# Performance work log

Hardware: AMD Instinct MI355X
Metric: run time of the kernel (lower is better)

The kernel has to match this reference:

```python
import jax, jax.numpy as jnp
import numpy as np

H = 128      # hidden_sizes
E = 128      # embedding_size
V = 100000   # n_words
C = 10       # n_classes
B, S, L = 32, 32, 64
PAD = 0


def _gru_dir(x, w_ih, w_hh, b_ih, b_hh, reverse):
    # x: [N, T, D]; torch GRU cell convention (r, z, n gate order)
    xp = jnp.einsum('ntd,gd->ntg', x, w_ih) + b_ih  # [N, T, 3H]
    if reverse:
        xp = xp[:, ::-1]
    h0 = jnp.zeros((x.shape[0], w_hh.shape[1]), x.dtype)

    def step(h, xt):
        gh = h @ w_hh.T + b_hh
        xr, xz, xn = jnp.split(xt, 3, axis=-1)
        hr, hz, hn = jnp.split(gh, 3, axis=-1)
        r = jax.nn.sigmoid(xr + hr)
        z = jax.nn.sigmoid(xz + hz)
        n = jnp.tanh(xn + r * hn)
        h2 = (1.0 - z) * n + z * h
        return h2, h2

    _, hs = jax.lax.scan(step, h0, jnp.swapaxes(xp, 0, 1))
    hs = jnp.swapaxes(hs, 0, 1)  # [N, T, H]
    if reverse:
        hs = hs[:, ::-1]
    return hs


def _bi_gru(x, pf, pb):
    return jnp.concatenate([_gru_dir(x, *pf, False), _gru_dir(x, *pb, True)], axis=-1)


def _attn_pool(h, W, b, ctx):
    # h: [N, T, 2H] -> pooled [N, 2H]
    u = jnp.tanh(jnp.einsum('ntd,ed->nte', h, W) + b)
    a = jax.nn.softmax(u @ ctx, axis=1)          # [N, T]
    return jnp.einsum('ntd,nt->nd', h, a)


def setup_inputs() -> dict:
    key = jax.random.key(0)
    ks = jax.random.split(key, 24)
    sc = 0.05
    d = {}
    d['X'] = jax.random.randint(ks[0], (B, S, L), 0, V, dtype=jnp.int32)
    d['emb'] = jax.random.normal(ks[1], (V, E), jnp.float32) * sc
    # word-level bi-GRU (input E)
    d['w_ih_f'] = jax.random.normal(ks[2], (3 * H, E), jnp.float32) * sc
    d['w_hh_f'] = jax.random.normal(ks[3], (3 * H, H), jnp.float32) * sc
    d['b_ih_f'] = jnp.zeros((3 * H,), jnp.float32)
    d['b_hh_f'] = jnp.zeros((3 * H,), jnp.float32)
    d['w_ih_b'] = jax.random.normal(ks[4], (3 * H, E), jnp.float32) * sc
    d['w_hh_b'] = jax.random.normal(ks[5], (3 * H, H), jnp.float32) * sc
    d['b_ih_b'] = jnp.zeros((3 * H,), jnp.float32)
    d['b_hh_b'] = jnp.zeros((3 * H,), jnp.float32)
    d['Ww'] = jax.random.normal(ks[6], (2 * H, 2 * H), jnp.float32) * sc
    d['bw'] = jnp.zeros((2 * H,), jnp.float32)
    d['ctx_w'] = jax.random.normal(ks[7], (2 * H,), jnp.float32) * sc
    # sentence-level bi-GRU (input 2H)
    d['s_ih_f'] = jax.random.normal(ks[8], (3 * H, 2 * H), jnp.float32) * sc
    d['s_hh_f'] = jax.random.normal(ks[9], (3 * H, H), jnp.float32) * sc
    d['sb_ih_f'] = jnp.zeros((3 * H,), jnp.float32)
    d['sb_hh_f'] = jnp.zeros((3 * H,), jnp.float32)
    d['s_ih_b'] = jax.random.normal(ks[10], (3 * H, 2 * H), jnp.float32) * sc
    d['s_hh_b'] = jax.random.normal(ks[11], (3 * H, H), jnp.float32) * sc
    d['sb_ih_b'] = jnp.zeros((3 * H,), jnp.float32)
    d['sb_hh_b'] = jnp.zeros((3 * H,), jnp.float32)
    d['Ws'] = jax.random.normal(ks[12], (2 * H, 2 * H), jnp.float32) * sc
    d['bs'] = jnp.zeros((2 * H,), jnp.float32)
    d['ctx_s'] = jax.random.normal(ks[13], (2 * H,), jnp.float32) * sc
    d['Wc'] = jax.random.normal(ks[14], (C, 2 * H), jnp.float32) * sc
    d['bc'] = jnp.zeros((C,), jnp.float32)
    return d


def reference(X, emb, w_ih_f, w_hh_f, b_ih_f, b_hh_f, w_ih_b, w_hh_b, b_ih_b, b_hh_b,
              Ww, bw, ctx_w, s_ih_f, s_hh_f, sb_ih_f, sb_hh_f, s_ih_b, s_hh_b,
              sb_ih_b, sb_hh_b, Ws, bs, ctx_s, Wc, bc):
    emb = emb.at[PAD].set(0.0)               # padding_idx semantics
    words = emb[X.reshape(B * S, L)]          # [B*S, L, E]
    h_w = _bi_gru(words, (w_ih_f, w_hh_f, b_ih_f, b_hh_f),
                  (w_ih_b, w_hh_b, b_ih_b, b_hh_b))  # [B*S, L, 2H]
    sents = _attn_pool(h_w, Ww, bw, ctx_w).reshape(B, S, 2 * H)
    h_s = _bi_gru(sents, (s_ih_f, s_hh_f, sb_ih_f, sb_hh_f),
                  (s_ih_b, s_hh_b, sb_ih_b, sb_hh_b))  # [B, S, 2H]
    doc = _attn_pool(h_s, Ws, bs, ctx_s)      # [B, 2H]
    return doc @ Wc.T + bc                    # [B, C]
```

## Files before the change

### kernel.cpp

```cpp
#include <hip/hip_runtime.h>
#include <hip/hip_bf16.h>
#include <math.h>

#define Bd 32
#define Sd 32
#define Ld 64
#define Ed 128
#define Hd 128
#define MW 65536
#define MS 1024

#define OFF_WIHT_S   0
#define OFF_WFW_W    196608
#define OFF_WFW_S    262144
#define OFF_W6       327680
#define OFF_BIH_W    622592
#define OFF_BIH_S    623360
#define OFF_BHH_W    624128
#define OFF_BHH_S    624896
#define OFF_WFX      625664
#define OFF_HW       723968
#define OFF_SENTS    17763328
#define OFF_XP_S     18025472
#define OFF_HS       18811904
#define OFF_DOC      19078144
#define OFF_WFHH     19086336
#define WS_FLOATS    19184640

typedef __attribute__((ext_vector_type(8))) short sh8;
typedef __attribute__((ext_vector_type(4))) float f32x4;
typedef unsigned short u16;
typedef unsigned int u32;

#define GLD  388
#define XPLD 385
#define HPLD 520

__device__ __forceinline__ void barrier_lds_only() {
    asm volatile("s_waitcnt lgkmcnt(0)\n\ts_barrier" ::: "memory");
}

__device__ __forceinline__ float sigmoidf_(float x) {
    return __fdividef(1.0f, 1.0f + __expf(-x));
}
__device__ __forceinline__ float tanhf_(float x) {
    float t = __expf(-2.0f * fabsf(x));
    float r = __fdividef(1.0f - t, 1.0f + t);
    return copysignf(r, x);
}
__device__ __forceinline__ u16 bf16_hi(float f) {
    u32 x = __float_as_uint(f);
    return (u16)((x + 0x7fffu + ((x >> 16) & 1u)) >> 16);
}
__device__ __forceinline__ float bf16_f(u16 u) { return __uint_as_float(((u32)u) << 16); }
__device__ __forceinline__ void bf16_split(float f, u16& hi, u16& lo) {
    hi = bf16_hi(f);
    lo = bf16_hi(f - bf16_f(hi));
}

__global__ void prep(const float* __restrict__ s_ih_f, const float* __restrict__ s_ih_b,
                     const float* __restrict__ w_ih_f, const float* __restrict__ w_ih_b,
                     const float* __restrict__ w_hh_f, const float* __restrict__ w_hh_b,
                     const float* __restrict__ s_hh_f, const float* __restrict__ s_hh_b,
                     const float* __restrict__ b_ih_f, const float* __restrict__ b_ih_b,
                     const float* __restrict__ sb_ih_f, const float* __restrict__ sb_ih_b,
                     const float* __restrict__ b_hh_f, const float* __restrict__ b_hh_b,
                     const float* __restrict__ sb_hh_f, const float* __restrict__ sb_hh_b,
                     float* __restrict__ ws)
{
    int i = blockIdx.x * 256 + threadIdx.x;
    if (i < 196608) {
        int k = i / 768, g = i % 768;
        ws[OFF_WIHT_S + i] = (g < 384) ? s_ih_f[g*256 + k] : s_ih_b[(g-384)*256 + k];
        return;
    }
    i -= 196608;
    if (i < 131072) return;
    i -= 131072;
    if (i < 294912) {
        int set = i / 49152, rem = i % 49152;
        int k4 = rem / 1536, r2 = rem % 1536, g = r2 >> 2, sub = r2 & 3;
        const float* w = (set==0) ? w_ih_f : (set==1) ? w_ih_b : (set==2) ? w_hh_f
                       : (set==3) ? w_hh_b : (set==4) ? s_hh_f : s_hh_b;
        ws[OFF_W6 + i] = w[g*128 + k4*4 + sub];
        return;
    }
    i -= 294912;
    if (i < 768) { ws[OFF_BIH_W + i] = (i<384) ? b_ih_f[i] : b_ih_b[i-384]; return; }
    i -= 768;
    if (i < 768) { ws[OFF_BIH_S + i] = (i<384) ? sb_ih_f[i] : sb_ih_b[i-384]; return; }
    i -= 768;
    if (i < 768) { ws[OFF_BHH_W + i] = (i<384) ? b_hh_f[i] : b_hh_b[i-384]; return; }
    i -= 768;
    if (i < 768) { ws[OFF_BHH_S + i] = (i<384) ? sb_hh_f[i] : sb_hh_b[i-384]; return; }
}

__global__ void prep2(const float* __restrict__ w_hh_f, const float* __restrict__ w_hh_b,
                      u16* __restrict__ WFo)
{
    int i = blockIdx.x * 256 + threadIdx.x;
    int within = i % 49152;
    int combo  = i / 49152;
    int half = combo & 1, dir = combo >> 1;
    int nt  = within / 2048;
    int r2  = within % 2048;
    int q   = r2 >> 9;
    int r3  = r2 & 511;
    int l   = r3 >> 3, e = r3 & 7;
    int n = nt*16 + (l & 15);
    int k = q*32 + ((l >> 4) << 3) + e;
    const float* src = dir ? w_hh_b : w_hh_f;
    float v = src[n*128 + k];
    u16 hi = bf16_hi(v);
    WFo[i] = half ? bf16_hi(v - bf16_f(hi)) : hi;
}

__global__ void prep3(const float* __restrict__ Ww, const float* __restrict__ Ws,
                      const float* __restrict__ w_ih_f, const float* __restrict__ w_ih_b,
                      u16* __restrict__ WFW_W, u16* __restrict__ WFW_S,
                      u16* __restrict__ WFX)
{
    int i = blockIdx.x * 256 + threadIdx.x;
    if (i < 262144) {
        int which = i / 131072;
        int w = i % 131072;
        int half = w / 65536;
        int r = w % 65536;
        int nt = r / 4096;
        int r2 = r % 4096;
        int q = r2 / 512;
        int l = (r2 % 512) >> 3, e = r2 & 7;
        int n = nt*16 + (l & 15);
        int k = q*32 + ((l >> 4) << 3) + e;
        const float* src = which ? Ws : Ww;
        float v = src[n*256 + k];
        u16 hi = bf16_hi(v);
        u16 o = half ? bf16_hi(v - bf16_f(hi)) : hi;
        (which ? WFW_S : WFW_W)[w] = o;
        return;
    }
    i -= 262144;
    if (i < 196608) {
        int w = i % 98304;
        int dir = i / 98304;
        int half = w / 49152;
        int r = w % 49152;
        int nt = r / 2048;
        int r2 = r % 2048;
        int q = r2 / 512;
        int l = (r2 % 512) >> 3, e = r2 & 7;
        int n = nt*16 + (l & 15);
        int k = q*32 + ((l >> 4) << 3) + e;
        const float* src = dir ? w_ih_b : w_ih_f;
        float v = src[n*128 + k];
        u16 hi = bf16_hi(v);
        WFX[i] = half ? bf16_hi(v - bf16_f(hi)) : hi;
        return;
    }
}

__global__ __launch_bounds__(768)
void gru_word_full(const int* __restrict__ X, const float* __restrict__ emb,
                   const u16* __restrict__ WFX, const u16* __restrict__ WFHH,
                   const float* __restrict__ b_ih_f, const float* __restrict__ b_ih_b,
                   const float* __restrict__ b_hh_f, const float* __restrict__ b_hh_b,
                   u16* __restrict__ houtp)
{
    const int bx = blockIdx.x;
    const int dir = bx >> 7;
    const int blk = bx & 127;
    const int seq0 = blk * 8;
    const int tid = threadIdx.x;
    const int lane = tid & 63;
    const int wid = tid >> 6;

    __shared__ float xp_lds[64 * XPLD];
    __shared__ f32x4 uni4[2048];
    __shared__ u16 h_pk[4 * HPLD];
    __shared__ int ids_s[8][64];
    float* G = (float*)uni4;
    u16* a_pk = (u16*)uni4;

    const int j = tid & 127;
    const int sg = tid >> 7;
    const bool gthread = tid < 512;
    const float* bih = dir ? b_ih_b : b_ih_f;
    const float* bhh = dir ? b_hh_b : b_hh_f;
    float bhr = 0.f, bhz = 0.f, bhn = 0.f;
    if (gthread) { bhr = bhh[j]; bhz = bhh[128 + j]; bhn = bhh[256 + j]; }

    const u16* WXbase = WFX + (long)dir * 98304;
    const u16* WHbase = WFHH + (long)dir * 98304;
    const int nt0 = wid*2, nt1 = wid*2 + 1;
    const int c0 = nt0*16 + (lane & 15);
    const int c1 = nt1*16 + (lane & 15);
    const int qj = j >> 5, subkj = (j >> 3) & 3, ej = j & 7;

    for (int i = tid; i < 512; i += 768)
        ids_s[i >> 6][i & 63] = X[(long)(seq0 + (i >> 6))*64 + (i & 63)];
    for (int i = tid; i < 4*HPLD; i += 768) h_pk[i] = 0;
    __syncthreads();

    float hprev0 = 0.f, hprev1 = 0.f;
    for (int c = 0; c < 8; ++c) {
        asm volatile("" ::: "memory");
        sh8 xh0[4], xl0[4], xh1[4], xl1[4];
#pragma unroll
        for (int q = 0; q < 4; ++q) {
            xh0[q] = *(const sh8*)(WXbase + (nt0*4 + q)*512 + lane*8);
            xl0[q] = *(const sh8*)(WXbase + 49152 + (nt0*4 + q)*512 + lane*8);
            xh1[q] = *(const sh8*)(WXbase + (nt1*4 + q)*512 + lane*8);
            xl1[q] = *(const sh8*)(WXbase + 49152 + (nt1*4 + q)*512 + lane*8);
        }
        const float bv0 = bih[c0], bv1 = bih[c1];
        for (int idx = tid; idx < 2048; idx += 768) {
            int cc2 = idx & 1, rm = (idx >> 1) & 7, subk = (idx >> 4) & 3;
            int q = (idx >> 6) & 3, mfs = idx >> 8;
            int ts = c*8 + rm;
            int t = dir ? 63 - ts : ts;
            int kk = q*32 + subk*8 + cc2*4;
            int id = ids_s[mfs][t];
            float4 v = make_float4(0.f, 0.f, 0.f, 0.f);
            if (id != 0) v = *(const float4*)&emb[(long)id*128 + kk];
            u16 h0,l0,h1,l1,h2,l2,h3,l3;
            bf16_split(v.x,h0,l0); bf16_split(v.y,h1,l1);
            bf16_split(v.z,h2,l2); bf16_split(v.w,h3,l3);
            int lh = subk*16 + rm;
            int base = (mfs*4 + q)*512 + lh*8 + cc2*4;
            uint2 whi = make_uint2((u32)h0 | ((u32)h1 << 16), (u32)h2 | ((u32)h3 << 16));
            uint2 wlo = make_uint2((u32)l0 | ((u32)l1 << 16), (u32)l2 | ((u32)l3 << 16));
            *(uint2*)&a_pk[base]      = whi;
            *(uint2*)&a_pk[base + 64] = wlo;
        }
        barrier_lds_only();
#pragma unroll
        for (int mf = 0; mf < 8; ++mf) {
            f32x4 A0 = (f32x4){0.f,0.f,0.f,0.f};
            f32x4 A1 = (f32x4){0.f,0.f,0.f,0.f};
#pragma unroll
            for (int q = 0; q < 4; ++q) {
                sh8 a = *(const sh8*)&a_pk[(mf*4 + q)*512 + lane*8];
                A0 = __builtin_amdgcn_mfma_f32_16x16x32_bf16(a, xh0[q], A0, 0,0,0);
                A0 = __builtin_amdgcn_mfma_f32_16x16x32_bf16(a, xl0[q], A0, 0,0,0);
                A1 = __builtin_amdgcn_mfma_f32_16x16x32_bf16(a, xh1[q], A1, 0,0,0);
                A1 = __builtin_amdgcn_mfma_f32_16x16x32_bf16(a, xl1[q], A1, 0,0,0);
            }
            float g0[4], g1[4];
#pragma unroll
            for (int r = 0; r < 4; ++r) {
                g0[r] = A0[r] + __shfl_xor(A0[r], 32);
                g1[r] = A1[r] + __shfl_xor(A1[r], 32);
            }
            if ((lane >= 32) == (mf & 1)) {
                int row = mf*8 + ((lane >> 4) & 1)*4;
#pragma unroll
                for (int r = 0; r < 4; ++r) {
                    xp_lds[(row+r)*XPLD + c0] = g0[r] + bv0;
                    xp_lds[(row+r)*XPLD + c1] = g1[r] + bv1;
                }
            }
        }
        barrier_lds_only();
        asm volatile("" ::: "memory");
        sh8 wh0[4], wl0[4], wh1[4], wl1[4];
#pragma unroll
        for (int q = 0; q < 4; ++q) {
            wh0[q] = *(const sh8*)(WHbase + (nt0*4 + q)*512 + lane*8);
            wl0[q] = *(const sh8*)(WHbase + 49152 + (nt0*4 + q)*512 + lane*8);
            wh1[q] = *(const sh8*)(WHbase + (nt1*4 + q)*512 + lane*8);
            wl1[q] = *(const sh8*)(WHbase + 49152 + (nt1*4 + q)*512 + lane*8);
        }
        for (int tt = 0; tt < 8; ++tt) {
            const int ts = c*8 + tt;
            const int t = dir ? 63 - ts : ts;
            f32x4 acc0 = (f32x4){0.f,0.f,0.f,0.f};
            f32x4 acc1 = (f32x4){0.f,0.f,0.f,0.f};
#pragma unroll
            for (int q = 0; q < 4; ++q) {
                sh8 hp = *(const sh8*)&h_pk[q*HPLD + lane*8];
                acc0 = __builtin_amdgcn_mfma_f32_16x16x32_bf16(hp, wh0[q], acc0, 0,0,0);
                acc0 = __builtin_amdgcn_mfma_f32_16x16x32_bf16(hp, wl0[q], acc0, 0,0,0);
                acc1 = __builtin_amdgcn_mfma_f32_16x16x32_bf16(hp, wh1[q], acc1, 0,0,0);
                acc1 = __builtin_amdgcn_mfma_f32_16x16x32_bf16(hp, wl1[q], acc1, 0,0,0);
            }
            {
                float sg0[4], sg1[4];
#pragma unroll
                for (int r = 0; r < 4; ++r) {
                    sg0[r] = acc0[r] + __shfl_xor(acc0[r], 32);
                    sg1[r] = acc1[r] + __shfl_xor(acc1[r], 32);
                }
                if (lane < 32) {
                    const int col16 = lane & 15;
                    const int row0  = (lane >> 4) << 2;
#pragma unroll
                    for (int r = 0; r < 4; ++r) {
                        G[(row0+r)*GLD + nt0*16 + col16] = sg0[r];
                        G[(row0+r)*GLD + nt1*16 + col16] = sg1[r];
                    }
                }
            }
            barrier_lds_only();
            if (gthread) {
#pragma unroll
                for (int si = 0; si < 2; ++si) {
                    const int s = sg + si*4;
                    float gr  = G[s*GLD + j]       + bhr;
                    float gz  = G[s*GLD + 128 + j] + bhz;
                    float gnh = G[s*GLD + 256 + j] + bhn;
                    const float* xrow = &xp_lds[(s*8 + tt)*XPLD];
                    float r  = sigmoidf_(xrow[j] + gr);
                    float z  = sigmoidf_(xrow[128 + j] + gz);
                    float nv = tanhf_(xrow[256 + j] + r * gnh);
                    float hold = si ? hprev1 : hprev0;
                    float hnew = (1.f - z) * nv + z * hold;
                    if (si) hprev1 = hnew; else hprev0 = hnew;
                    u16 hh, hl; bf16_split(hnew, hh, hl);
                    u16 ohh = (u16)__shfl_xor((int)hh, 1);
                    u16 ohl = (u16)__shfl_xor((int)hl, 1);
                    const long tbase = ((long)(seq0 + s)*64 + t)*512 + dir*128;
                    if ((j & 1) == 0) {
                        u32 w = (u32)hh | ((u32)ohh << 16);
                        *(u32*)&h_pk[qj*HPLD + (subkj*16 + s)*8 + ej] = w;
                        *(u32*)&houtp[tbase + j] = w;
                    } else {
                        u32 w = (u32)ohl | ((u32)hl << 16);
                        *(u32*)&h_pk[qj*HPLD + (subkj*16 + s + 8)*8 + (ej - 1)] = w;
                        *(u32*)&houtp[tbase + 256 + (j - 1)] = w;
                    }
                }
            }
            barrier_lds_only();
        }
    }
}

template<int T, bool PACKED>
__global__ __launch_bounds__(1024)
void attn_fused(const float* __restrict__ A, const u16* __restrict__ WF,
                const float* __restrict__ bias, const float* __restrict__ ctx,
                float* __restrict__ outp)
{
    __shared__ u16 a_pk[8][8][512];
    __shared__ float pscore[8][8][17];
    __shared__ float aw[64];
    __shared__ float red[4][256];
    const int tid = threadIdx.x;
    const int lane = tid & 63;
    const int wid = tid >> 6;
    const int m0 = blockIdx.x * 64;

    sh8 bh[8], bl[8];
#pragma unroll
    for (int q = 0; q < 8; ++q) {
        bh[q] = *(const sh8*)(WF + (wid*8 + q)*512 + lane*8);
        bl[q] = *(const sh8*)(WF + 65536 + (wid*8 + q)*512 + lane*8);
    }
    const int colg = wid*16 + (lane & 15);
    const float bwv = bias[colg];
    const float cxv = ctx[colg];

    if (PACKED) {
        const u32* src32 = (const u32*)A + (long)blockIdx.x * 16384;
        u32* dst = (u32*)a_pk;
        for (int idx = tid; idx < 16384; idx += 1024) {
            int mf = idx >> 11, q = (idx >> 8) & 7, l = (idx >> 2) & 63, c2 = idx & 3;
            int row16 = l & 15, hilo = row16 >> 3, rm = row16 & 7;
            int t = mf*8 + rm;
            int k = q*32 + (l >> 4)*8 + c2*2;
            dst[idx] = src32[(t*2 + hilo)*128 + (k >> 1)];
        }
    } else {
        for (int idx = tid; idx < 8192; idx += 1024) {
            int row = idx >> 7;
            int k   = (idx & 127) << 1;
            float2 v = *(const float2*)&A[(long)(m0 + row)*256 + k];
            u16 h0,l0,h1,l1; bf16_split(v.x,h0,l0); bf16_split(v.y,h1,l1);
            int mf = row >> 3, rm = row & 7;
            int q = k >> 5;
            int lh = (((k & 31) >> 3) << 4) | rm;
            int e = k & 7;
            *(u32*)&a_pk[mf][q][lh*8 + e]     = (u32)h0 | ((u32)h1 << 16);
            *(u32*)&a_pk[mf][q][(lh+8)*8 + e] = (u32)l0 | ((u32)l1 << 16);
        }
    }
    __syncthreads();

#pragma unroll
    for (int mf = 0; mf < 8; ++mf) {
        f32x4 acc = (f32x4){0.f,0.f,0.f,0.f};
#pragma unroll
        for (int q = 0; q < 8; ++q) {
            sh8 a = *(const sh8*)&a_pk[mf][q][lane*8];
            acc = __builtin_amdgcn_mfma_f32_16x16x32_bf16(a, bh[q], acc, 0,0,0);
            acc = __builtin_amdgcn_mfma_f32_16x16x32_bf16(a, bl[q], acc, 0,0,0);
        }
        float g[4];
#pragma unroll
        for (int r = 0; r < 4; ++r) g[r] = acc[r] + __shfl_xor(acc[r], 32);
        if ((lane >= 32) == (mf & 1)) {
            float p[4];
#pragma unroll
            for (int r = 0; r < 4; ++r) p[r] = tanhf_(g[r] + bwv) * cxv;
#pragma unroll
            for (int r = 0; r < 4; ++r) {
                p[r] += __shfl_xor(p[r], 1);
                p[r] += __shfl_xor(p[r], 2);
                p[r] += __shfl_xor(p[r], 4);
                p[r] += __shfl_xor(p[r], 8);
            }
            if ((lane & 15) == 0) {
#pragma unroll
                for (int r = 0; r < 4; ++r)
                    pscore[mf][((lane >> 4) & 1)*4 + r][wid] = p[r];
            }
        }
    }
    __syncthreads();

    if (tid < 64) {
        float sc = 0.f;
#pragma unroll
        for (int w = 0; w < 16; ++w) sc += pscore[tid >> 3][tid & 7][w];
        float mx = sc;
#pragma unroll
        for (int m = 1; m < T; m <<= 1) mx = fmaxf(mx, __shfl_xor(mx, m));
        float e = __expf(sc - mx);
        float den = e;
#pragma unroll
        for (int m = 1; m < T; m <<= 1) den += __shfl_xor(den, m);
        aw[tid] = __fdividef(e, den);
    }
    __syncthreads();

    if (tid < 512) {
        const int dp = (tid & 127) << 1;
        const int tg = tid >> 7;
        const int q = dp >> 5, lhb = ((dp & 31) >> 3) << 4, e = dp & 7;
        float acc0 = 0.f, acc1 = 0.f;
#pragma unroll
        for (int i = 0; i < 16; ++i) {
            int t = tg*16 + i;
            int mf = t >> 3, rm = t & 7;
            const u16* base = &a_pk[mf][q][(lhb | rm)*8 + e];
            u32 hh = *(const u32*)base;
            u32 ll = *(const u32*)(base + 64);
            float h0 = bf16_f((u16)hh) + bf16_f((u16)ll);
            float h1 = bf16_f((u16)(hh >> 16)) + bf16_f((u16)(ll >> 16));
            float w = aw[t];
            acc0 = fmaf(w, h0, acc0);
            acc1 = fmaf(w, h1, acc1);
        }
        red[tg][dp] = acc0; red[tg][dp + 1] = acc1;
    }
    __syncthreads();
    if (T == 64) {
        if (tid < 256)
            outp[(long)blockIdx.x*256 + tid] = red[0][tid] + red[1][tid] + red[2][tid] + red[3][tid];
    } else {
        if (tid < 512) {
            int sent = tid >> 8, dd = tid & 255;
            outp[((long)blockIdx.x*2 + sent)*256 + dd] = red[sent*2][dd] + red[sent*2 + 1][dd];
        }
    }
}

__global__ __launch_bounds__(256)
void gemm_xp(const float* __restrict__ A,
             const float* __restrict__ WT, const float* __restrict__ bias,
             float* __restrict__ out, int N, int K)
{
    __shared__ float As[64*128];
    __shared__ float Bs[128*64];
    const int tid = threadIdx.x;
    const int m0 = blockIdx.x * 64;
    const int n0 = blockIdx.y * 64;
    const int tx = tid & 15, ty = tid >> 4;
    float acc[4][4];
#pragma unroll
    for (int i=0;i<4;i++)
#pragma unroll
        for (int c=0;c<4;c++) acc[i][c]=0.f;

    for (int kc = 0; kc < K; kc += 128) {
        if (kc) __syncthreads();
#pragma unroll
        for (int it = 0; it < 8; ++it) {
            int idx = tid + it*256;
            int r = idx >> 5, c4 = idx & 31;
            float4 v = *(const float4*)&A[(long)(m0 + r)*K + kc + (c4<<2)];
            *(float4*)&As[r*128 + ((c4 ^ (r & 7)) << 2)] = v;
        }
#pragma unroll
        for (int it = 0; it < 8; ++it) {
            int idx = tid + it*256;
            int k = idx >> 4, c4 = idx & 15;
            float4 v = *(const float4*)&WT[(long)(kc + k)*N + n0 + (c4<<2)];
            *(float4*)&Bs[k*64 + ((c4 ^ (k & 7)) << 2)] = v;
        }
        __syncthreads();
        const int swzA = (ty & 7) << 2;
#pragma unroll 4
        for (int k = 0; k < 128; ++k) {
            float4 b = *(const float4*)&Bs[k*64 + ((tx ^ (k & 7)) << 2)];
            int kx = k ^ swzA;
#pragma unroll
            for (int i=0;i<4;i++) {
                float a = As[(ty + 16*i)*128 + kx];
                acc[i][0] = fmaf(a, b.x, acc[i][0]);
                acc[i][1] = fmaf(a, b.y, acc[i][1]);
                acc[i][2] = fmaf(a, b.z, acc[i][2]);
                acc[i][3] = fmaf(a, b.w, acc[i][3]);
            }
        }
    }
    float4 bia = *(const float4*)&bias[n0 + (tx<<2)];
#pragma unroll
    for (int i=0;i<4;i++) {
        float4 res = make_float4(acc[i][0]+bia.x, acc[i][1]+bia.y, acc[i][2]+bia.z, acc[i][3]+bia.w);
        *(float4*)&out[(long)(m0 + ty + 16*i)*N + n0 + (tx<<2)] = res;
    }
}

template<int NSEQ, int T>
__global__ __launch_bounds__(512)
void gru_fused(const float* __restrict__ xp, const float4* __restrict__ whh4,
               const float* __restrict__ bhh, float* __restrict__ hout,
               int blocks_per_dir)
{
    const int bx = blockIdx.x;
    const int dir = bx / blocks_per_dir;
    const int blk = bx % blocks_per_dir;
    const int seq0 = blk * NSEQ;
    const int tid = threadIdx.x;
    const int kq = tid & 3;
    const int j  = tid >> 2;
    const float4* W = whh4 + (long)dir * 12288;
    __shared__ float h_lds[NSEQ][128];
    for (int idx = tid; idx < NSEQ*128; idx += 512) ((float*)h_lds)[idx] = 0.f;
    const float bhr = bhh[dir*384 + j];
    const float bhz = bhh[dir*384 + 128 + j];
    const float bhn = bhh[dir*384 + 256 + j];
    __syncthreads();

    for (int ts = 0; ts < T; ++ts) {
        const int t = dir ? (T - 1 - ts) : ts;
        float a0[NSEQ], a1[NSEQ], a2[NSEQ];
#pragma unroll
        for (int s=0;s<NSEQ;s++){a0[s]=0.f;a1[s]=0.f;a2[s]=0.f;}
#pragma unroll
        for (int ii = 0; ii < 8; ++ii) {
            const int k4 = kq + (ii << 2);
            float4 w0 = W[k4*384 + j];
            float4 w1 = W[k4*384 + 128 + j];
            float4 w2 = W[k4*384 + 256 + j];
#pragma unroll
            for (int s=0;s<NSEQ;s++) {
                float4 h4 = *(const float4*)&h_lds[s][k4 << 2];
                a0[s] = fmaf(w0.x,h4.x, fmaf(w0.y,h4.y, fmaf(w0.z,h4.z, fmaf(w0.w,h4.w, a0[s]))));
                a1[s] = fmaf(w1.x,h4.x, fmaf(w1.y,h4.y, fmaf(w1.z,h4.z, fmaf(w1.w,h4.w, a1[s]))));
                a2[s] = fmaf(w2.x,h4.x, fmaf(w2.y,h4.y, fmaf(w2.z,h4.z, fmaf(w2.w,h4.w, a2[s]))));
            }
        }
#pragma unroll
        for (int s=0;s<NSEQ;s++) {
            a0[s] += __shfl_xor(a0[s], 1); a0[s] += __shfl_xor(a0[s], 2);
            a1[s] += __shfl_xor(a1[s], 1); a1[s] += __shfl_xor(a1[s], 2);
            a2[s] += __shfl_xor(a2[s], 1); a2[s] += __shfl_xor(a2[s], 2);
        }
        __syncthreads();
        if (kq == 0) {
#pragma unroll
            for (int s=0;s<NSEQ;s++) {
                const float* xr = &xp[((long)(seq0+s)*T + t)*768 + dir*384];
                float r = sigmoidf_(xr[j]       + a0[s] + bhr);
                float z = sigmoidf_(xr[128 + j] + a1[s] + bhz);
                float nv = tanhf_(xr[256 + j] + r * (a2[s] + bhn));
                float hold = h_lds[s][j];
                float hnew = (1.f - z) * nv + z * hold;
                h_lds[s][j] = hnew;
                hout[((long)(seq0+s)*T + t)*256 + dir*128 + j] = hnew;
            }
        }
        __syncthreads();
    }
}

__global__ void classifier(const float* __restrict__ doc, const float* __restrict__ Wc,
                           const float* __restrict__ bc, float* __restrict__ out)
{
    int tid = threadIdx.x;
    if (tid < 320) {
        int b = tid / 10, c = tid % 10;
        float s = bc[c];
        for (int d = 0; d < 256; ++d) s = fmaf(doc[b*256 + d], Wc[c*256 + d], s);
        out[tid] = s;
    }
}

extern "C" void kernel_launch(void* const* d_in, const int* in_sizes, int n_in,
                              void* d_out, int out_size, void* d_ws, size_t ws_size,
                              hipStream_t stream) {
    const int*   X       = (const int*)  d_in[0];
    const float* emb     = (const float*)d_in[1];
    const float* w_ih_f  = (const float*)d_in[2];
    const float* w_hh_f  = (const float*)d_in[3];
    const float* b_ih_f  = (const float*)d_in[4];
    const float* b_hh_f  = (const float*)d_in[5];
    const float* w_ih_b  = (const float*)d_in[6];
    const float* w_hh_b  = (const float*)d_in[7];
    const float* b_ih_b  = (const float*)d_in[8];
    const float* b_hh_b  = (const float*)d_in[9];
    const float* Ww      = (const float*)d_in[10];
    const float* bw      = (const float*)d_in[11];
    const float* ctx_w   = (const float*)d_in[12];
    const float* s_ih_f  = (const float*)d_in[13];
    const float* s_hh_f  = (const float*)d_in[14];
    const float* sb_ih_f = (const float*)d_in[15];
    const float* sb_hh_f = (const float*)d_in[16];
    const float* s_ih_b  = (const float*)d_in[17];
    const float* s_hh_b  = (const float*)d_in[18];
    const float* sb_ih_b = (const float*)d_in[19];
    const float* sb_hh_b = (const float*)d_in[20];
    const float* Ws      = (const float*)d_in[21];
    const float* bs      = (const float*)d_in[22];
    const float* ctx_s   = (const float*)d_in[23];
    const float* Wc      = (const float*)d_in[24];
    const float* bc      = (const float*)d_in[25];
    float* ws  = (float*)d_ws;
    float* out = (float*)d_out;

    if (ws_size < (size_t)WS_FLOATS * 4) return;

    prep<<<2444, 256, 0, stream>>>(s_ih_f, s_ih_b, w_ih_f, w_ih_b,
                                   w_hh_f, w_hh_b, s_hh_f, s_hh_b,
                                   b_ih_f, b_ih_b, sb_ih_f, sb_ih_b,
                                   b_hh_f, b_hh_b, sb_hh_f, sb_hh_b, ws);
    prep2<<<768, 256, 0, stream>>>(w_hh_f, w_hh_b, (u16*)(ws + OFF_WFHH));
    prep3<<<1792, 256, 0, stream>>>(Ww, Ws, w_ih_f, w_ih_b,
                                    (u16*)(ws + OFF_WFW_W), (u16*)(ws + OFF_WFW_S),
                                    (u16*)(ws + OFF_WFX));

    gru_word_full<<<256, 768, 0, stream>>>(
        X, emb, (const u16*)(ws + OFF_WFX), (const u16*)(ws + OFF_WFHH),
        b_ih_f, b_ih_b, b_hh_f, b_hh_b, (u16*)(ws + OFF_HW));

    attn_fused<64, true><<<1024, 1024, 0, stream>>>(
        ws + OFF_HW, (const u16*)(ws + OFF_WFW_W), bw, ctx_w, ws + OFF_SENTS);

    gemm_xp<<<dim3(16, 12), 256, 0, stream>>>(
        ws + OFF_SENTS, ws + OFF_WIHT_S, ws + OFF_BIH_S, ws + OFF_XP_S, 768, 256);
    gru_fused<1, 32><<<64, 512, 0, stream>>>(
        ws + OFF_XP_S, (const float4*)(ws + OFF_W6) + 4*12288, ws + OFF_BHH_S, ws + OFF_HS, 32);
    attn_fused<32, false><<<16, 1024, 0, stream>>>(
        ws + OFF_HS, (const u16*)(ws + OFF_WFW_S), bs, ctx_s, ws + OFF_DOC);
    classifier<<<1, 320, 0, stream>>>(ws + OFF_DOC, Wc, bc, out);
}
```

Baseline: 351.3 us.

## Merge prep kernels, prefetch xp in GRU step, hoist weights to registers

Merges the three weight-preparation kernels into one launch, removing two kernel launches and the gaps between them. In the word GRU, the precomputed input projections are loaded from LDS before the MFMA step so their latency overlaps the matrix work. In the sentence GRU, the recurrent weight float4s are hoisted into registers once instead of being reloaded every timestep. The classifier is also vectorised with float4 loads. The register hoisting raises register pressure and may lower occupancy.

```diff
diff --git a/kernel.cpp b/kernel.cpp
--- a/kernel.cpp
+++ b/kernel.cpp
@@ -58,104 +58,106 @@
     lo = bf16_hi(f - bf16_f(hi));
 }
 
-__global__ void prep(const float* __restrict__ s_ih_f, const float* __restrict__ s_ih_b,
-                     const float* __restrict__ w_ih_f, const float* __restrict__ w_ih_b,
-                     const float* __restrict__ w_hh_f, const float* __restrict__ w_hh_b,
-                     const float* __restrict__ s_hh_f, const float* __restrict__ s_hh_b,
-                     const float* __restrict__ b_ih_f, const float* __restrict__ b_ih_b,
-                     const float* __restrict__ sb_ih_f, const float* __restrict__ sb_ih_b,
-                     const float* __restrict__ b_hh_f, const float* __restrict__ b_hh_b,
-                     const float* __restrict__ sb_hh_f, const float* __restrict__ sb_hh_b,
-                     float* __restrict__ ws)
+__global__ void prep_all(const float* __restrict__ s_ih_f, const float* __restrict__ s_ih_b,
+                         const float* __restrict__ w_ih_f, const float* __restrict__ w_ih_b,
+                         const float* __restrict__ w_hh_f, const float* __restrict__ w_hh_b,
+                         const float* __restrict__ s_hh_f, const float* __restrict__ s_hh_b,
+                         const float* __restrict__ b_ih_f, const float* __restrict__ b_ih_b,
+                         const float* __restrict__ sb_ih_f, const float* __restrict__ sb_ih_b,
+                         const float* __restrict__ b_hh_f, const float* __restrict__ b_hh_b,
+                         const float* __restrict__ sb_hh_f, const float* __restrict__ sb_hh_b,
+                         const float* __restrict__ Ww, const float* __restrict__ Ws,
+                         float* __restrict__ ws)
 {
-    int i = blockIdx.x * 256 + threadIdx.x;
-    if (i < 196608) {
-        int k = i / 768, g = i % 768;
-        ws[OFF_WIHT_S + i] = (g < 384) ? s_ih_f[g*256 + k] : s_ih_b[(g-384)*256 + k];
+    const int b = blockIdx.x;
+    if (b < 2444) {
+        int i = b * 256 + threadIdx.x;
+        if (i < 196608) {
+            int k = i / 768, g = i % 768;
+            ws[OFF_WIHT_S + i] = (g < 384) ? s_ih_f[g*256 + k] : s_ih_b[(g-384)*256 + k];
+            return;
+        }
+        i -= 196608;
+        if (i < 131072) return;
+        i -= 131072;
+        if (i < 294912) {
+            int set = i / 49152, rem = i % 49152;
+            int k4 = rem / 1536, r2 = rem % 1536, g = r2 >> 2, sub = r2 & 3;
+            const float* w = (set==0) ? w_ih_f : (set==1) ? w_ih_b : (set==2) ? w_hh_f
+                           : (set==3) ? w_hh_b : (set==4) ? s_hh_f : s_hh_b;
+            ws[OFF_W6 + i] = w[g*128 + k4*4 + sub];
+            return;
+        }
+        i -= 294912;
+        if (i < 768) { ws[OFF_BIH_W + i] = (i<384) ? b_ih_f[i] : b_ih_b[i-384]; return; }
+        i -= 768;
+        if (i < 768) { ws[OFF_BIH_S + i] = (i<384) ? sb_ih_f[i] : sb_ih_b[i-384]; return; }
+        i -= 768;
+        if (i < 768) { ws[OFF_BHH_W + i] = (i<384) ? b_hh_f[i] : b_hh_b[i-384]; return; }
+        i -= 768;
+        if (i < 768) { ws[OFF_BHH_S + i] = (i<384) ? sb_hh_f[i] : sb_hh_b[i-384]; return; }
         return;
     }
-    i -= 196608;
-    if (i < 131072) return;
-    i -= 131072;
-    if (i < 294912) {
-        int set = i / 49152, rem = i % 49152;
-        int k4 = rem / 1536, r2 = rem % 1536, g = r2 >> 2, sub = r2 & 3;
-        const float* w = (set==0) ? w_ih_f : (set==1) ? w_ih_b : (set==2) ? w_hh_f
-                       : (set==3) ? w_hh_b : (set==4) ? s_hh_f : s_hh_b;
-        ws[OFF_W6 + i] = w[g*128 + k4*4 + sub];
-        return;
-    }
-    i -= 294912;
-    if (i < 768) { ws[OFF_BIH_W + i] = (i<384) ? b_ih_f[i] : b_ih_b[i-384]; return; }
-    i -= 768;
-    if (i < 768) { ws[OFF_BIH_S + i] = (i<384) ? sb_ih_f[i] : sb_ih_b[i-384]; return; }
-    i -= 768;
-    if (i < 768) { ws[OFF_BHH_W + i] = (i<384) ? b_hh_f[i] : b_hh_b[i-384]; return; }
-    i -= 768;
-    if (i < 768) { ws[OFF_BHH_S + i] = (i<384) ? sb_hh_f[i] : sb_hh_b[i-384]; return; }
-}
-
-__global__ void prep2(const float* __restrict__ w_hh_f, const float* __restrict__ w_hh_b,
-                      u16* __restrict__ WFo)
-{
-    int i = blockIdx.x * 256 + threadIdx.x;
-    int within = i % 49152;
-    int combo  = i / 49152;
-    int half = combo & 1, dir = combo >> 1;
-    int nt  = within / 2048;
-    int r2  = within % 2048;
-    int q   = r2 >> 9;
-    int r3  = r2 & 511;
-    int l   = r3 >> 3, e = r3 & 7;
-    int n = nt*16 + (l & 15);
-    int k = q*32 + ((l >> 4) << 3) + e;
-    const float* src = dir ? w_hh_b : w_hh_f;
-    float v = src[n*128 + k];
-    u16 hi = bf16_hi(v);
-    WFo[i] = half ? bf16_hi(v - bf16_f(hi)) : hi;
-}
-
-__global__ void prep3(const float* __restrict__ Ww, const float* __restrict__ Ws,
-                      const float* __restrict__ w_ih_f, const float* __restrict__ w_ih_b,
-                      u16* __restrict__ WFW_W, u16* __restrict__ WFW_S,
-                      u16* __restrict__ WFX)
-{
-    int i = blockIdx.x * 256 + threadIdx.x;
-    if (i < 262144) {
-        int which = i / 131072;
-        int w = i % 131072;
-        int half = w / 65536;
-        int r = w % 65536;
-        int nt = r / 4096;
-        int r2 = r % 4096;
-        int q = r2 / 512;
-        int l = (r2 % 512) >> 3, e = r2 & 7;
+    if (b < 3212) {
+        u16* WFo = (u16*)(ws + OFF_WFHH);
+        int i = (b - 2444) * 256 + threadIdx.x;
+        int within = i % 49152;
+        int combo  = i / 49152;
+        int half = combo & 1, dir = combo >> 1;
+        int nt  = within / 2048;
+        int r2  = within % 2048;
+        int q   = r2 >> 9;
+        int r3  = r2 & 511;
+        int l   = r3 >> 3, e = r3 & 7;
         int n = nt*16 + (l & 15);
         int k = q*32 + ((l >> 4) << 3) + e;
-        const float* src = which ? Ws : Ww;
-        float v = src[n*256 + k];
-        u16 hi = bf16_hi(v);
-        u16 o = half ? bf16_hi(v - bf16_f(hi)) : hi;
-        (which ? WFW_S : WFW_W)[w] = o;
-        return;
-    }
-    i -= 262144;
-    if (i < 196608) {
-        int w = i % 98304;
-        int dir = i / 98304;
-        int half = w / 49152;
-        int r = w % 49152;
-        int nt = r / 2048;
-        int r2 = r % 2048;
-        int q = r2 / 512;
-        int l = (r2 % 512) >> 3, e = r2 & 7;
-        int n = nt*16 + (l & 15);
-        int k = q*32 + ((l >> 4) << 3) + e;
-        const float* src = dir ? w_ih_b : w_ih_f;
+        const float* src = dir ? w_hh_b : w_hh_f;
         float v = src[n*128 + k];
         u16 hi = bf16_hi(v);
-        WFX[i] = half ? bf16_hi(v - bf16_f(hi)) : hi;
+        WFo[i] = half ? bf16_hi(v - bf16_f(hi)) : hi;
         return;
+    }
+    {
+        u16* WFW_W = (u16*)(ws + OFF_WFW_W);
+        u16* WFW_S = (u16*)(ws + OFF_WFW_S);
+        u16* WFX   = (u16*)(ws + OFF_WFX);
+        int i = (b - 3212) * 256 + threadIdx.x;
+        if (i < 262144) {
+            int which = i / 131072;
+            int w = i % 131072;
+            int half = w / 65536;
+            int r = w % 65536;
+            int nt = r / 4096;
+            int r2 = r % 4096;
+            int q = r2 / 512;
+            int l = (r2 % 512) >> 3, e = r2 & 7;
+            int n = nt*16 + (l & 15);
+            int k = q*32 + ((l >> 4) << 3) + e;
+            const float* src = which ? Ws : Ww;
+            float v = src[n*256 + k];
+            u16 hi = bf16_hi(v);
+            u16 o = half ? bf16_hi(v - bf16_f(hi)) : hi;
+            (which ? WFW_S : WFW_W)[w] = o;
+            return;
+        }
+        i -= 262144;
+        if (i < 196608) {
+            int w = i % 98304;
+            int dir = i / 98304;
+            int half = w / 49152;
+            int r = w % 49152;
+            int nt = r / 2048;
+            int r2 = r % 2048;
+            int q = r2 / 512;
+            int l = (r2 % 512) >> 3, e = r2 & 7;
+            int n = nt*16 + (l & 15);
+            int k = q*32 + ((l >> 4) << 3) + e;
+            const float* src = dir ? w_ih_b : w_ih_f;
+            float v = src[n*128 + k];
+            u16 hi = bf16_hi(v);
+            WFX[i] = half ? bf16_hi(v - bf16_f(hi)) : hi;
+            return;
+        }
     }
 }
 
@@ -273,6 +275,16 @@
         for (int tt = 0; tt < 8; ++tt) {
             const int ts = c*8 + tt;
             const int t = dir ? 63 - ts : ts;
+            float pxr[2], pxz[2], pxn[2];
+            if (gthread) {
+#pragma unroll
+                for (int si = 0; si < 2; ++si) {
+                    const float* xrow = &xp_lds[((sg + si*4)*8 + tt)*XPLD];
+                    pxr[si] = xrow[j];
+                    pxz[si] = xrow[128 + j];
+                    pxn[si] = xrow[256 + j];
+                }
+            }
             f32x4 acc0 = (f32x4){0.f,0.f,0.f,0.f};
             f32x4 acc1 = (f32x4){0.f,0.f,0.f,0.f};
 #pragma unroll
@@ -308,10 +320,9 @@
                     float gr  = G[s*GLD + j]       + bhr;
                     float gz  = G[s*GLD + 128 + j] + bhz;
                     float gnh = G[s*GLD + 256 + j] + bhn;
-                    const float* xrow = &xp_lds[(s*8 + tt)*XPLD];
-                    float r  = sigmoidf_(xrow[j] + gr);
-                    float z  = sigmoidf_(xrow[128 + j] + gz);
-                    float nv = tanhf_(xrow[256 + j] + r * gnh);
+                    float r  = sigmoidf_(pxr[si] + gr);
+                    float z  = sigmoidf_(pxz[si] + gz);
+                    float nv = tanhf_(pxn[si] + r * gnh);
                     float hold = si ? hprev1 : hprev0;
                     float hnew = (1.f - z) * nv + z * hold;
                     if (si) hprev1 = hnew; else hprev0 = hnew;
@@ -541,6 +552,14 @@
     const float bhr = bhh[dir*384 + j];
     const float bhz = bhh[dir*384 + 128 + j];
     const float bhn = bhh[dir*384 + 256 + j];
+    float4 w0r[8], w1r[8], w2r[8];
+#pragma unroll
+    for (int ii = 0; ii < 8; ++ii) {
+        const int k4 = kq + (ii << 2);
+        w0r[ii] = W[k4*384 + j];
+        w1r[ii] = W[k4*384 + 128 + j];
+        w2r[ii] = W[k4*384 + 256 + j];
+    }
     __syncthreads();
 
     for (int ts = 0; ts < T; ++ts) {
@@ -551,9 +570,9 @@
 #pragma unroll
         for (int ii = 0; ii < 8; ++ii) {
             const int k4 = kq + (ii << 2);
-            float4 w0 = W[k4*384 + j];
-            float4 w1 = W[k4*384 + 128 + j];
-            float4 w2 = W[k4*384 + 256 + j];
+            float4 w0 = w0r[ii];
+            float4 w1 = w1r[ii];
+            float4 w2 = w2r[ii];
 #pragma unroll
             for (int s=0;s<NSEQ;s++) {
                 float4 h4 = *(const float4*)&h_lds[s][k4 << 2];
@@ -593,7 +612,12 @@
     if (tid < 320) {
         int b = tid / 10, c = tid % 10;
         float s = bc[c];
-        for (int d = 0; d < 256; ++d) s = fmaf(doc[b*256 + d], Wc[c*256 + d], s);
+        const float4* dp = (const float4*)&doc[b*256];
+        const float4* wp = (const float4*)&Wc[c*256];
+        for (int d = 0; d < 64; ++d) {
+            float4 a = dp[d], w = wp[d];
+            s = fmaf(a.x, w.x, fmaf(a.y, w.y, fmaf(a.z, w.z, fmaf(a.w, w.w, s))));
+        }
         out[tid] = s;
     }
 }
@@ -632,14 +656,11 @@
 
     if (ws_size < (size_t)WS_FLOATS * 4) return;
 
-    prep<<<2444, 256, 0, stream>>>(s_ih_f, s_ih_b, w_ih_f, w_ih_b,
-                                   w_hh_f, w_hh_b, s_hh_f, s_hh_b,
-                                   b_ih_f, b_ih_b, sb_ih_f, sb_ih_b,
-                                   b_hh_f, b_hh_b, sb_hh_f, sb_hh_b, ws);
-    prep2<<<768, 256, 0, stream>>>(w_hh_f, w_hh_b, (u16*)(ws + OFF_WFHH));
-    prep3<<<1792, 256, 0, stream>>>(Ww, Ws, w_ih_f, w_ih_b,
-                                    (u16*)(ws + OFF_WFW_W), (u16*)(ws + OFF_WFW_S),
-                                    (u16*)(ws + OFF_WFX));
+    prep_all<<<5004, 256, 0, stream>>>(s_ih_f, s_ih_b, w_ih_f, w_ih_b,
+                                       w_hh_f, w_hh_b, s_hh_f, s_hh_b,
+                                       b_ih_f, b_ih_b, sb_ih_f, sb_ih_b,
+                                       b_hh_f, b_hh_b, sb_hh_f, sb_hh_b,
+                                       Ww, Ws, ws);
 
     gru_word_full<<<256, 768, 0, stream>>>(
         X, emb, (const u16*)(ws + OFF_WFX), (const u16*)(ws + OFF_WFHH),
```

Measured after the change: 335.1 us. 1.05x faster.
